# Optimization experiments

Hardware: AMD Instinct MI355X
Metric: run time of the kernel (lower is better)

The kernel has to match this reference:

```python
import jax, jax.numpy as jnp
import numpy as np

C_FEAT = 64


def _dilation_indices(seq_len, dilation):
    # Static (trace-time) replication of _generate_dilation_mask, as index set.
    side = int(round(seq_len ** (1.0 / 3.0)))  # 32 for N=32768
    g = np.arange(side)
    zz, yy, xx = np.meshgrid(g, g, g, indexing='ij')
    coords = np.stack([zz, yy, xx], axis=-1).astype(np.float32)
    center = side // 2
    d = np.sqrt(((coords - center) ** 2).sum(-1))
    mask = ((d % dilation) == 0) | (d == 0)
    return jnp.asarray(np.nonzero(mask.reshape(-1))[0], dtype=jnp.int32)


def _dst_block(x, qkv_w, qkv_b, proj_w, proj_b, idx):
    # x: [B, N, C]; attention restricted to the dilation-sampled token subset.
    B, N, C = x.shape
    qkv = x @ qkv_w.T + qkv_b                      # [B, N, 3C]
    q, k, v = jnp.split(qkv, 3, axis=-1)           # each [B, N, C]
    qs, ks, vs = q[:, idx], k[:, idx], v[:, idx]   # [B, M, C] (gather == dense-then-mask)
    scale = 1.0 / jnp.sqrt(jnp.asarray(C, x.dtype))
    attn = jax.nn.softmax(jnp.einsum('bmc,bnc->bmn', qs, ks) * scale, axis=-1)
    y = jnp.einsum('bmn,bnc->bmc', attn, vs)       # [B, M, C]
    out = (y @ proj_w.T + proj_b) + y              # proj + residual
    # scatter sampled tokens back so the token grid stays N (see notes)
    return x.at[:, idx].set(out)


def _lerp_axis(x, axis, out_size):
    # 1-D linear interp along `axis`, align_corners=True
    n = x.shape[axis]
    pos = jnp.arange(out_size, dtype=jnp.float32) * ((n - 1) / (out_size - 1))
    i0 = jnp.floor(pos).astype(jnp.int32)
    i1 = jnp.minimum(i0 + 1, n - 1)
    w = pos - i0.astype(jnp.float32)
    shp = [1] * x.ndim
    shp[axis] = out_size
    w = w.reshape(shp)
    return jnp.take(x, i0, axis=axis) * (1.0 - w) + jnp.take(x, i1, axis=axis) * w


def _forward(x, w_patch, b_patch, pos_embed,
             qkv_w1, qkv_b1, proj_w1, proj_b1,
             qkv_w2, qkv_b2, proj_w2, proj_b2,
             qkv_w3, qkv_b3, proj_w3, proj_b3):
    h = jax.lax.conv_general_dilated(
        x, w_patch, window_strides=(4, 4, 4), padding='VALID',
        dimension_numbers=('NCDHW', 'OIDHW', 'NCDHW'))
    h = h + b_patch[None, :, None, None, None]          # [B, C, 32, 32, 32]
    B, C, Z, Y, X = h.shape
    N = Z * Y * X
    t = h.reshape(B, C, N).transpose(0, 2, 1)
    t = t + pos_embed.reshape(1, C, N).transpose(0, 2, 1)
    for (qw, qb, pw, pb, dil) in ((qkv_w1, qkv_b1, proj_w1, proj_b1, 2),
                                  (qkv_w2, qkv_b2, proj_w2, proj_b2, 4),
                                  (qkv_w3, qkv_b3, proj_w3, proj_b3, 6)):
        idx = _dilation_indices(N, dil)
        t = _dst_block(t, qw, qb, pw, pb, idx)
    h = t.transpose(0, 2, 1).reshape(B, C, Z, Y, X)
    # trilinear upsample x4, align_corners=True
    for ax in (2, 3, 4):
        h = _lerp_axis(h, ax, h.shape[ax] * 4)
    return h


def setup_inputs() -> dict:
    key = jax.random.key(0)
    ks = jax.random.split(key, 12)
    C = C_FEAT
    d = {
        'x': jax.random.normal(ks[0], (1, 1, 128, 128, 128), jnp.float32),
        'w_patch': jax.random.normal(ks[1], (C, 1, 4, 4, 4), jnp.float32) * 0.1,
        'b_patch': jnp.zeros((C,), jnp.float32),
        'pos_embed': jax.random.normal(ks[2], (1, C, 32, 32, 32), jnp.float32) * 0.02,
    }
    for i in range(3):
        d[f'qkv_w{i+1}'] = jax.random.normal(ks[3 + 3 * i], (3 * C, C), jnp.float32) * 0.05
        d[f'qkv_b{i+1}'] = jnp.zeros((3 * C,), jnp.float32)
        d[f'proj_w{i+1}'] = jax.random.normal(ks[4 + 3 * i], (C, C), jnp.float32) * 0.05
        d[f'proj_b{i+1}'] = jnp.zeros((C,), jnp.float32)
    return d


def reference(x, w_patch, b_patch, pos_embed,
              qkv_w1, qkv_b1, proj_w1, proj_b1,
              qkv_w2, qkv_b2, proj_w2, proj_b2,
              qkv_w3, qkv_b3, proj_w3, proj_b3):
    return _forward(x, w_patch, b_patch, pos_embed,
                    qkv_w1, qkv_b1, proj_w1, proj_b1,
                    qkv_w2, qkv_b2, proj_w2, proj_b2,
                    qkv_w3, qkv_b3, proj_w3, proj_b3)
```

## Files before the change

kernel.cpp:

```cpp
#include <hip/hip_runtime.h>
#include <cmath>

#define NTOK 32768
#define CF   64

__global__ void patch_kernel(const float* __restrict__ x,
                             const float* __restrict__ w,
                             const float* __restrict__ bias,
                             const float* __restrict__ pos,
                             float* __restrict__ t) {
    __shared__ float xsT[64 * 32];
    __shared__ float wT[64 * 65];
    int tid = threadIdx.x;
    int z = blockIdx.x >> 5, y = blockIdx.x & 31;

    for (int k = tid; k < 4096; k += 256) {
        int c = k >> 6, tap = k & 63;
        wT[tap * 65 + c] = w[k];
    }
    #pragma unroll
    for (int p = 0; p < 2; ++p) {
        int q = tid + p * 256;
        int r = q >> 5;
        int col4 = q & 31;
        int dz = r >> 2, dy = r & 3;
        const float4* src = (const float4*)(x + (size_t)((z * 4 + dz) * 128 + (y * 4 + dy)) * 128);
        float4 v = src[col4];
        int tb = dz * 16 + dy * 4;
        xsT[(tb + 0) * 32 + col4] = v.x;
        xsT[(tb + 1) * 32 + col4] = v.y;
        xsT[(tb + 2) * 32 + col4] = v.z;
        xsT[(tb + 3) * 32 + col4] = v.w;
    }
    __syncthreads();

    int xx = tid & 31;
    int ch = tid >> 5;
    int n = z * 1024 + y * 32 + xx;
    #pragma unroll
    for (int p = 0; p < 8; ++p) {
        int c = ch + p * 8;
        float acc = bias[c];
        #pragma unroll
        for (int k = 0; k < 64; ++k)
            acc += xsT[k * 32 + xx] * wT[k * 65 + c];
        t[c * NTOK + n] = acc + pos[c * NTOK + n];
    }
}

__global__ void qkv_kernel(const float* __restrict__ t,
                           const float* __restrict__ w,
                           const float* __restrict__ bias,
                           const int* __restrict__ idx,
                           float* __restrict__ qkv) {
    __shared__ float tv[64];
    __shared__ float ws[192 * 65];
    int i = blockIdx.x, j = threadIdx.x;
    int n = idx[i];
    if (j < 64) tv[j] = t[j * NTOK + n];
    for (int k = j; k < 12288; k += 192)
        ws[(k >> 6) * 65 + (k & 63)] = w[k];
    __syncthreads();
    float acc = bias[j];
    const float* wr = ws + j * 65;
    #pragma unroll
    for (int c = 0; c < 64; ++c) acc += tv[c] * wr[c];
    qkv[i * 192 + j] = acc;
}

__global__ void attn_proj_kernel(const float* __restrict__ qkv,
                                 float* __restrict__ t,
                                 const float* __restrict__ pw,
                                 const float* __restrict__ pb,
                                 const int* __restrict__ idx,
                                 int M) {
    __shared__ float qs[64];
    __shared__ float yv[64];
    __shared__ float p[512];
    __shared__ float pwt[64 * 65];
    int i = blockIdx.x, lane = threadIdx.x;
    qs[lane] = qkv[i * 192 + lane];
    for (int k = lane; k < 4096; k += 64)
        pwt[(k & 63) * 65 + (k >> 6)] = pw[k];
    __syncthreads();

    const float scale = 0.125f;
    for (int j = lane; j < M; j += 64) {
        const float4* kr = (const float4*)(qkv + j * 192 + 64);
        float acc = 0.f;
        #pragma unroll
        for (int c4 = 0; c4 < 16; ++c4) {
            float4 kv = kr[c4];
            acc += qs[c4 * 4 + 0] * kv.x + qs[c4 * 4 + 1] * kv.y
                 + qs[c4 * 4 + 2] * kv.z + qs[c4 * 4 + 3] * kv.w;
        }
        p[j] = acc * scale;
    }
    __syncthreads();
    float m = -INFINITY;
    for (int j = lane; j < M; j += 64) m = fmaxf(m, p[j]);
    #pragma unroll
    for (int off = 32; off > 0; off >>= 1) m = fmaxf(m, __shfl_xor(m, off));
    float s = 0.f;
    for (int j = lane; j < M; j += 64) { float e = expf(p[j] - m); p[j] = e; s += e; }
    #pragma unroll
    for (int off = 32; off > 0; off >>= 1) s += __shfl_xor(s, off);
    __syncthreads();
    float inv = 1.f / s;
    float acc = 0.f;
    for (int j = 0; j < M; ++j)
        acc += p[j] * qkv[j * 192 + 128 + lane];
    float yc = acc * inv;
    yv[lane] = yc;
    __syncthreads();
    float facc = pb[lane] + yc;
    #pragma unroll
    for (int q = 0; q < 64; ++q)
        facc += yv[q] * pwt[q * 65 + lane];
    t[lane * NTOK + idx[i]] = facc;
}

__global__ void upsample_kernel(const float* __restrict__ h, float* __restrict__ out) {
    int bc = blockIdx.x;
    int c = bc >> 7, zo = bc & 127;
    __shared__ float pz[1024];
    __shared__ float wtab[128];
    __shared__ int   itab[128];
    int tid = threadIdx.x;
    const float scale = (float)(31.0 / 127.0);
    if (tid < 128) {
        float p = (float)tid * scale;
        int i0 = (int)floorf(p);
        if (i0 > 31) i0 = 31;
        itab[tid] = i0;
        wtab[tid] = p - (float)i0;
    }
    float pzf = (float)zo * scale;
    int zi0 = (int)floorf(pzf);
    if (zi0 > 31) zi0 = 31;
    int zi1 = min(zi0 + 1, 31);
    float wz = pzf - (float)zi0;
    const float4* pl0 = (const float4*)(h + (c * 32 + zi0) * 1024);
    const float4* pl1 = (const float4*)(h + (c * 32 + zi1) * 1024);
    float4 a = pl0[tid];
    float4 b = pl1[tid];
    float4 r;
    r.x = a.x * (1.f - wz) + b.x * wz;
    r.y = a.y * (1.f - wz) + b.y * wz;
    r.z = a.z * (1.f - wz) + b.z * wz;
    r.w = a.w * (1.f - wz) + b.w * wz;
    ((float4*)pz)[tid] = r;
    __syncthreads();
    float4* o = (float4*)(out + (size_t)(c * 128 + zo) * 16384);
    for (int q = 0; q < 16; ++q) {
        int Q = q * 256 + tid;
        int yo = Q >> 5, xq = Q & 31;
        int yi0 = itab[yo];
        float wy = wtab[yo];
        int yi1 = min(yi0 + 1, 31);
        const float* r0 = pz + yi0 * 32;
        const float* r1 = pz + yi1 * 32;
        float vv[4];
        #pragma unroll
        for (int k = 0; k < 4; ++k) {
            int xo = xq * 4 + k;
            int xi0 = itab[xo];
            float wx = wtab[xo];
            int xi1 = min(xi0 + 1, 31);
            float v0 = r0[xi0] * (1.f - wx) + r0[xi1] * wx;
            float v1 = r1[xi0] * (1.f - wx) + r1[xi1] * wx;
            vv[k] = v0 * (1.f - wy) + v1 * wy;
        }
        float4 v; v.x = vv[0]; v.y = vv[1]; v.z = vv[2]; v.w = vv[3];
        o[Q] = v;
    }
}

extern "C" void kernel_launch(void* const* d_in, const int* in_sizes, int n_in,
                              void* d_out, int out_size, void* d_ws, size_t ws_size,
                              hipStream_t stream) {
    const float* x       = (const float*)d_in[0];
    const float* w_patch = (const float*)d_in[1];
    const float* b_patch = (const float*)d_in[2];
    const float* pos     = (const float*)d_in[3];
    const float* qkv_w[3]  = {(const float*)d_in[4],  (const float*)d_in[8],  (const float*)d_in[12]};
    const float* qkv_b[3]  = {(const float*)d_in[5],  (const float*)d_in[9],  (const float*)d_in[13]};
    const float* proj_w[3] = {(const float*)d_in[6],  (const float*)d_in[10], (const float*)d_in[14]};
    const float* proj_b[3] = {(const float*)d_in[7],  (const float*)d_in[11], (const float*)d_in[15]};
    float* out = (float*)d_out;

    char* ws = (char*)d_ws;
    if (ws_size < (size_t)(16u << 20)) return;
    float* t   = (float*)ws;
    float* qkv = (float*)(ws + (8u << 20));
    int*   idx = (int*)  (ws + (9u << 20));

    static int h_idx[3 * 1024];
    int M[3];
    for (int di = 0; di < 3; ++di) {
        int dil = 2 * (di + 1), cnt = 0;
        for (int n = 0; n < NTOK; ++n) {
            int z = n >> 10, yy = (n >> 5) & 31, xx = n & 31;
            int a = z - 16, b = yy - 16, c = xx - 16;
            int dd = a * a + b * b + c * c;
            int s = (int)(std::sqrt((double)dd) + 0.5);
            if (s * s == dd && (s % dil) == 0) h_idx[di * 1024 + cnt++] = n;
        }
        M[di] = cnt;
    }
    hipMemcpyAsync(idx, h_idx, sizeof(h_idx), hipMemcpyHostToDevice, stream);

    patch_kernel<<<1024, 256, 0, stream>>>(x, w_patch, b_patch, pos, t);
    for (int di = 0; di < 3; ++di) {
        qkv_kernel<<<M[di], 192, 0, stream>>>(t, qkv_w[di], qkv_b[di], idx + di * 1024, qkv);
        attn_proj_kernel<<<M[di], 64, 0, stream>>>(qkv, t, proj_w[di], proj_b[di], idx + di * 1024, M[di]);
    }
    upsample_kernel<<<CF * 128, 256, 0, stream>>>(t, out);
}
```

Measured before the change: 721.9 us.

## Fold QKV and projection weights algebraically into fused attention kernel with token tiles

Precomputes folded matrices (Wk^T Wq scaled, (Wp+I)Wv, plus bias terms) in a small prep kernel so the attention works directly on raw token features. A single fused kernel loads all sampled tokens into LDS, computes scores via the folded bilinear form, runs softmax, and applies the folded value/projection. Patch embedding now writes both token-major and channel-major copies so the gather is coalesced, and a scatter kernel updates both. This removes the separate QKV projection kernel and the per-block weight reloads, at the cost of extra writes and an LDS footprint that caps sampled tokens at 280.

```diff
diff --git a/kernel.cpp b/kernel.cpp
--- a/kernel.cpp
+++ b/kernel.cpp
@@ -3,14 +3,74 @@
 
 #define NTOK 32768
 #define CF   64
-
-__global__ void patch_kernel(const float* __restrict__ x,
+#define TSP  66
+
+__global__ void prep_kernel(const float* __restrict__ qw0, const float* __restrict__ qb0,
+                            const float* __restrict__ pw0, const float* __restrict__ pb0,
+                            const float* __restrict__ qw1, const float* __restrict__ qb1,
+                            const float* __restrict__ pw1, const float* __restrict__ pb1,
+                            const float* __restrict__ qw2, const float* __restrict__ qb2,
+                            const float* __restrict__ pw2, const float* __restrict__ pb2,
+                            float* __restrict__ consts) {
+    int di = blockIdx.x;
+    const float* qw = di == 0 ? qw0 : (di == 1 ? qw1 : qw2);
+    const float* qb = di == 0 ? qb0 : (di == 1 ? qb1 : qb2);
+    const float* pw = di == 0 ? pw0 : (di == 1 ? pw1 : pw2);
+    const float* pb = di == 0 ? pb0 : (di == 1 ? pb1 : pb2);
+    float* base = consts + di * 8448;
+    float* At  = base;
+    float* Bt  = base + 4096;
+    float* bqp = base + 8192;
+    float* w2  = base + 8256;
+    float* bb  = base + 8320;
+    float* c0  = base + 8384;
+    int tid = threadIdx.x;
+    const float scale = 0.125f;
+    for (int o = tid; o < 4096; o += 256) {
+        int k = o >> 6, c = o & 63;
+        float a = 0.f;
+        for (int m = 0; m < 64; ++m)
+            a += qw[(64 + m) * 64 + c] * qw[m * 64 + k];
+        At[k * 64 + c] = scale * a;
+    }
+    for (int o = tid; o < 4096; o += 256) {
+        int c = o >> 6, k = o & 63;
+        float b = 0.f;
+        for (int m = 0; m < 64; ++m) {
+            float pp = pw[c * 64 + m] + (c == m ? 1.f : 0.f);
+            b += pp * qw[(128 + m) * 64 + k];
+        }
+        Bt[k * 64 + c] = b;
+    }
+    if (tid < 64) {
+        int c = tid;
+        float a = 0.f, w = 0.f, b = 0.f;
+        for (int m = 0; m < 64; ++m) {
+            a += qw[(64 + m) * 64 + c] * qb[m];
+            w += qb[64 + m] * qw[m * 64 + c];
+            float pp = pw[c * 64 + m] + (c == m ? 1.f : 0.f);
+            b += pp * qb[128 + m];
+        }
+        bqp[c] = scale * a;
+        w2[c]  = scale * w;
+        bb[c]  = b + pb[c];
+        if (c == 0) {
+            float s = 0.f;
+            for (int m = 0; m < 64; ++m) s += qb[m] * qb[64 + m];
+            c0[0] = scale * s;
+        }
+    }
+}
+
+__global__ __launch_bounds__(256) void patch_kernel(const float* __restrict__ x,
                              const float* __restrict__ w,
                              const float* __restrict__ bias,
                              const float* __restrict__ pos,
-                             float* __restrict__ t) {
+                             float* __restrict__ tnc,
+                             float* __restrict__ tcn) {
     __shared__ float xsT[64 * 32];
     __shared__ float wT[64 * 65];
+    __shared__ float res[64 * 33];
     int tid = threadIdx.x;
     int z = blockIdx.x >> 5, y = blockIdx.x & 31;
 
@@ -36,7 +96,7 @@
 
     int xx = tid & 31;
     int ch = tid >> 5;
-    int n = z * 1024 + y * 32 + xx;
+    int nb = z * 1024 + y * 32;
     #pragma unroll
     for (int p = 0; p < 8; ++p) {
         int c = ch + p * 8;
@@ -44,80 +104,117 @@
         #pragma unroll
         for (int k = 0; k < 64; ++k)
             acc += xsT[k * 32 + xx] * wT[k * 65 + c];
-        t[c * NTOK + n] = acc + pos[c * NTOK + n];
-    }
-}
-
-__global__ void qkv_kernel(const float* __restrict__ t,
-                           const float* __restrict__ w,
-                           const float* __restrict__ bias,
+        res[c * 33 + xx] = acc + pos[c * NTOK + nb + xx];
+    }
+    __syncthreads();
+    for (int q = tid; q < 2048; q += 256) {
+        int tok = q >> 6, c = q & 63;
+        tnc[(size_t)(nb + tok) * 64 + c] = res[c * 33 + tok];
+    }
+    for (int q = tid; q < 2048; q += 256) {
+        int c = q >> 5, x2 = q & 31;
+        tcn[(size_t)c * NTOK + nb + x2] = res[c * 33 + x2];
+    }
+}
+
+__global__ __launch_bounds__(256) void dst_kernel(const float* __restrict__ tnc,
+                           const float* __restrict__ cbase,
                            const int* __restrict__ idx,
-                           float* __restrict__ qkv) {
-    __shared__ float tv[64];
-    __shared__ float ws[192 * 65];
-    int i = blockIdx.x, j = threadIdx.x;
+                           float* __restrict__ yout, int M) {
+    __shared__ float ts[280 * TSP];
+    __shared__ float kqs[4 * 64];
+    const float* At  = cbase;
+    const float* Bt  = cbase + 4096;
+    const float* bqp = cbase + 8192;
+    const float* w2v = cbase + 8256;
+    const float* bbv = cbase + 8320;
+    const float* c0v = cbase + 8384;
+    int tid = threadIdx.x;
+    for (int q = tid; q < M * 16; q += 256) {
+        int j = q >> 4, c4 = (q & 15) << 2;
+        const float4 v = *(const float4*)(tnc + (size_t)idx[j] * 64 + c4);
+        float* d = ts + j * TSP + c4;
+        d[0] = v.x; d[1] = v.y; d[2] = v.z; d[3] = v.w;
+    }
+    __syncthreads();
+    int w = tid >> 6, lane = tid & 63;
+    int qi = blockIdx.x * 4 + w;
+    if (qi >= M) return;
+    const float* trow = ts + qi * TSP;
+    float kq = bqp[lane];
+    #pragma unroll 16
+    for (int k = 0; k < 64; ++k)
+        kq += At[k * 64 + lane] * trow[k];
+    kqs[w * 64 + lane] = kq;
+    float sb = w2v[lane] * trow[lane];
+    #pragma unroll
+    for (int off = 32; off > 0; off >>= 1) sb += __shfl_xor(sb, off);
+    sb += c0v[0];
+
+    float p[5];
+    float mx = -INFINITY;
+    const float2* kq2 = (const float2*)(kqs + w * 64);
+    #pragma unroll
+    for (int it = 0; it < 5; ++it) {
+        int j = it * 64 + lane;
+        p[it] = -INFINITY;
+        if (j < M) {
+            const float2* tr2 = (const float2*)(ts + j * TSP);
+            float s = sb;
+            #pragma unroll 8
+            for (int c = 0; c < 32; ++c) {
+                float2 a = kq2[c]; float2 b = tr2[c];
+                s += a.x * b.x + a.y * b.y;
+            }
+            p[it] = s; mx = fmaxf(mx, s);
+        }
+    }
+    #pragma unroll
+    for (int off = 32; off > 0; off >>= 1) mx = fmaxf(mx, __shfl_xor(mx, off));
+    float ssum = 0.f;
+    #pragma unroll
+    for (int it = 0; it < 5; ++it) {
+        int j = it * 64 + lane;
+        float e = (j < M) ? expf(p[it] - mx) : 0.f;
+        p[it] = e; ssum += e;
+    }
+    #pragma unroll
+    for (int off = 32; off > 0; off >>= 1) ssum += __shfl_xor(ssum, off);
+    float inv = 1.f / ssum;
+
+    float u = 0.f;
+    #pragma unroll
+    for (int it = 0; it < 5; ++it) {
+        int jb = it * 64;
+        if (jb < M) {
+            int cnt = min(64, M - jb);
+            for (int jj = 0; jj < cnt; ++jj) {
+                float pj = __shfl(p[it], jj);
+                u += pj * ts[(jb + jj) * TSP + lane];
+            }
+        }
+    }
+    u *= inv;
+    kqs[w * 64 + lane] = u;
+    float o = bbv[lane];
+    const float2* u2 = (const float2*)(kqs + w * 64);
+    #pragma unroll 8
+    for (int k = 0; k < 32; ++k) {
+        float2 uu = u2[k];
+        o += Bt[(2 * k) * 64 + lane] * uu.x + Bt[(2 * k + 1) * 64 + lane] * uu.y;
+    }
+    yout[qi * 64 + lane] = o;
+}
+
+__global__ void scatter_kernel(const float* __restrict__ yout,
+                               float* __restrict__ tnc,
+                               float* __restrict__ tcn,
+                               const int* __restrict__ idx) {
+    int i = blockIdx.x, c = threadIdx.x;
     int n = idx[i];
-    if (j < 64) tv[j] = t[j * NTOK + n];
-    for (int k = j; k < 12288; k += 192)
-        ws[(k >> 6) * 65 + (k & 63)] = w[k];
-    __syncthreads();
-    float acc = bias[j];
-    const float* wr = ws + j * 65;
-    #pragma unroll
-    for (int c = 0; c < 64; ++c) acc += tv[c] * wr[c];
-    qkv[i * 192 + j] = acc;
-}
-
-__global__ void attn_proj_kernel(const float* __restrict__ qkv,
-                                 float* __restrict__ t,
-                                 const float* __restrict__ pw,
-                                 const float* __restrict__ pb,
-                                 const int* __restrict__ idx,
-                                 int M) {
-    __shared__ float qs[64];
-    __shared__ float yv[64];
-    __shared__ float p[512];
-    __shared__ float pwt[64 * 65];
-    int i = blockIdx.x, lane = threadIdx.x;
-    qs[lane] = qkv[i * 192 + lane];
-    for (int k = lane; k < 4096; k += 64)
-        pwt[(k & 63) * 65 + (k >> 6)] = pw[k];
-    __syncthreads();
-
-    const float scale = 0.125f;
-    for (int j = lane; j < M; j += 64) {
-        const float4* kr = (const float4*)(qkv + j * 192 + 64);
-        float acc = 0.f;
-        #pragma unroll
-        for (int c4 = 0; c4 < 16; ++c4) {
-            float4 kv = kr[c4];
-            acc += qs[c4 * 4 + 0] * kv.x + qs[c4 * 4 + 1] * kv.y
-                 + qs[c4 * 4 + 2] * kv.z + qs[c4 * 4 + 3] * kv.w;
-        }
-        p[j] = acc * scale;
-    }
-    __syncthreads();
-    float m = -INFINITY;
-    for (int j = lane; j < M; j += 64) m = fmaxf(m, p[j]);
-    #pragma unroll
-    for (int off = 32; off > 0; off >>= 1) m = fmaxf(m, __shfl_xor(m, off));
-    float s = 0.f;
-    for (int j = lane; j < M; j += 64) { float e = expf(p[j] - m); p[j] = e; s += e; }
-    #pragma unroll
-    for (int off = 32; off > 0; off >>= 1) s += __shfl_xor(s, off);
-    __syncthreads();
-    float inv = 1.f / s;
-    float acc = 0.f;
-    for (int j = 0; j < M; ++j)
-        acc += p[j] * qkv[j * 192 + 128 + lane];
-    float yc = acc * inv;
-    yv[lane] = yc;
-    __syncthreads();
-    float facc = pb[lane] + yc;
-    #pragma unroll
-    for (int q = 0; q < 64; ++q)
-        facc += yv[q] * pwt[q * 65 + lane];
-    t[lane * NTOK + idx[i]] = facc;
+    float v = yout[i * 64 + c];
+    tnc[(size_t)n * 64 + c] = v;
+    tcn[(size_t)c * NTOK + n] = v;
 }
 
 __global__ void upsample_kernel(const float* __restrict__ h, float* __restrict__ out) {
@@ -183,17 +280,15 @@
     const float* w_patch = (const float*)d_in[1];
     const float* b_patch = (const float*)d_in[2];
     const float* pos     = (const float*)d_in[3];
-    const float* qkv_w[3]  = {(const float*)d_in[4],  (const float*)d_in[8],  (const float*)d_in[12]};
-    const float* qkv_b[3]  = {(const float*)d_in[5],  (const float*)d_in[9],  (const float*)d_in[13]};
-    const float* proj_w[3] = {(const float*)d_in[6],  (const float*)d_in[10], (const float*)d_in[14]};
-    const float* proj_b[3] = {(const float*)d_in[7],  (const float*)d_in[11], (const float*)d_in[15]};
     float* out = (float*)d_out;
 
     char* ws = (char*)d_ws;
-    if (ws_size < (size_t)(16u << 20)) return;
-    float* t   = (float*)ws;
-    float* qkv = (float*)(ws + (8u << 20));
-    int*   idx = (int*)  (ws + (9u << 20));
+    if (ws_size < (size_t)(20u << 20)) return;
+    float* tcn    = (float*)ws;
+    float* tnc    = (float*)(ws + (8u << 20));
+    float* yout   = (float*)(ws + (16u << 20));
+    int*   idx    = (int*)  (ws + (17u << 20));
+    float* consts = (float*)(ws + (18u << 20));
 
     static int h_idx[3 * 1024];
     int M[3];
@@ -210,10 +305,15 @@
     }
     hipMemcpyAsync(idx, h_idx, sizeof(h_idx), hipMemcpyHostToDevice, stream);
 
-    patch_kernel<<<1024, 256, 0, stream>>>(x, w_patch, b_patch, pos, t);
+    prep_kernel<<<3, 256, 0, stream>>>(
+        (const float*)d_in[4],  (const float*)d_in[5],  (const float*)d_in[6],  (const float*)d_in[7],
+        (const float*)d_in[8],  (const float*)d_in[9],  (const float*)d_in[10], (const float*)d_in[11],
+        (const float*)d_in[12], (const float*)d_in[13], (const float*)d_in[14], (const float*)d_in[15],
+        consts);
+    patch_kernel<<<1024, 256, 0, stream>>>(x, w_patch, b_patch, pos, tnc, tcn);
     for (int di = 0; di < 3; ++di) {
-        qkv_kernel<<<M[di], 192, 0, stream>>>(t, qkv_w[di], qkv_b[di], idx + di * 1024, qkv);
-        attn_proj_kernel<<<M[di], 64, 0, stream>>>(qkv, t, proj_w[di], proj_b[di], idx + di * 1024, M[di]);
-    }
-    upsample_kernel<<<CF * 128, 256, 0, stream>>>(t, out);
-}
+        dst_kernel<<<(M[di] + 3) / 4, 256, 0, stream>>>(tnc, consts + di * 8448, idx + di * 1024, yout, M[di]);
+        scatter_kernel<<<M[di], 64, 0, stream>>>(yout, tnc, tcn, idx + di * 1024);
+    }
+    upsample_kernel<<<CF * 128, 256, 0, stream>>>(tcn, out);
+}
```

Result: no change. 721.6 us (-0.0%).
